# Kernel optimization log

Measured on AMD Instinct MI355X. Metric: run time of the kernel, lower is better.

Reference implementation:

```python
import jax, jax.numpy as jnp
import numpy as np

EPS = 1e-6


def layernorm(x, g, b):
    m = jnp.mean(x, axis=-1, keepdims=True)
    v = jnp.var(x, axis=-1, keepdims=True)
    return (x - m) * jax.lax.rsqrt(v + EPS) * g + b


def dwconv(x, w, b):
    # x: (B,H,W,C), w: (kh,kw,1,C) depthwise kernel, SAME padding (stride 1)
    y = jax.lax.conv_general_dilated(
        x, w, window_strides=(1, 1), padding='SAME',
        dimension_numbers=('NHWC', 'HWIO', 'NHWC'),
        feature_group_count=x.shape[-1])
    return y + b


def setup_inputs() -> dict:
    key = jax.random.key(0)
    ks = jax.random.split(key, 16)
    B, H, W, C = 16, 64, 64, 256
    N, F = 8, 1024
    s = 0.02
    return {
        'x': jax.random.normal(ks[0], (B, H, W, C), jnp.float32),
        'mask_h': jax.random.normal(ks[1], (N, H, H), jnp.float32),
        'mask_w': jax.random.normal(ks[2], (N, W, W), jnp.float32),
        'pos_w': jax.random.normal(ks[3], (3, 3, 1, C), jnp.float32) * s,
        'pos_b': jnp.zeros((C,), jnp.float32),
        'ln1_g': jnp.ones((C,), jnp.float32),
        'ln1_b': jnp.zeros((C,), jnp.float32),
        'wq': jax.random.normal(ks[4], (C, C), jnp.float32) * s,
        'bq': jnp.zeros((C,), jnp.float32),
        'wk': jax.random.normal(ks[5], (C, C), jnp.float32) * s,
        'bk': jnp.zeros((C,), jnp.float32),
        'wv': jax.random.normal(ks[6], (C, C), jnp.float32) * s,
        'bv': jnp.zeros((C,), jnp.float32),
        'lepe_w': jax.random.normal(ks[7], (5, 5, 1, C), jnp.float32) * s,
        'lepe_b': jnp.zeros((C,), jnp.float32),
        'wo': jax.random.normal(ks[8], (C, C), jnp.float32) * s,
        'bo': jnp.zeros((C,), jnp.float32),
        'ln2_g': jnp.ones((C,), jnp.float32),
        'ln2_b': jnp.zeros((C,), jnp.float32),
        'fc1_w': jax.random.normal(ks[9], (C, F), jnp.float32) * s,
        'fc1_b': jnp.zeros((F,), jnp.float32),
        'fc2_w': jax.random.normal(ks[10], (F, C), jnp.float32) * s,
        'fc2_b': jnp.zeros((C,), jnp.float32),
    }


NUM_HEADS = 8


def masad(x, mask_h, mask_w, wq, bq, wk, bk, wv, bv, lepe_w, lepe_b, wo, bo):
    # x: (B,H,W,C); decomposed axial retention (MaSAd)
    B, H, W, C = x.shape
    n = NUM_HEADS
    d = C // n
    scaling = d ** (-0.5)
    q = x @ wq + bq
    k = (x @ wk + bk) * scaling
    v = x @ wv + bv
    lepe = dwconv(v, lepe_w, lepe_b)  # (B,H,W,C)
    q5 = q.reshape(B, H, W, n, d)
    k5 = k.reshape(B, H, W, n, d)
    v5 = v.reshape(B, H, W, n, d)
    # --- W-axis attention: scores (B,H,n,W,W)
    qk_w = jnp.einsum('bhqnd,bhknd->bhnqk', q5, k5)
    Aw = jax.nn.softmax(qk_w + mask_w[None, None], axis=-1)
    vo = jnp.einsum('bhnqk,bhknd->bhqnd', Aw, v5)  # (B,H,W,n,d)
    # --- H-axis attention: scores (B,W,n,H,H)
    qk_h = jnp.einsum('bqwnd,bkwnd->bwnqk', q5, k5)
    Ah = jax.nn.softmax(qk_h + mask_h[None, None], axis=-1)
    out = jnp.einsum('bwnqk,bkwnd->bqwnd', Ah, vo)  # (B,H,W,n,d)
    out = out.reshape(B, H, W, C) + lepe
    return out @ wo + bo


def reference(x, mask_h, mask_w, pos_w, pos_b, ln1_g, ln1_b,
              wq, bq, wk, bk, wv, bv, lepe_w, lepe_b, wo, bo,
              ln2_g, ln2_b, fc1_w, fc1_b, fc2_w, fc2_b):
    x = x + dwconv(x, pos_w, pos_b)
    x = x + masad(layernorm(x, ln1_g, ln1_b), mask_h, mask_w,
                  wq, bq, wk, bk, wv, bv, lepe_w, lepe_b, wo, bo)
    h = layernorm(x, ln2_g, ln2_b)
    h = jax.nn.gelu(h @ fc1_w + fc1_b, approximate=False)
    x = x + (h @ fc2_w + fc2_b)
    return x
```

## Files before the change

kernel.cpp:

```cpp
#include <hip/hip_runtime.h>
#include <hip/hip_bf16.h>
#include <math.h>

typedef unsigned short u16;
typedef unsigned int   u32;
typedef float f4   __attribute__((ext_vector_type(4)));
typedef float f32x4 __attribute__((ext_vector_type(4)));
typedef __bf16 bf16x8 __attribute__((ext_vector_type(8)));

#define BDIM 16
#define HDIM 64
#define WDIM 64
#define CDIM 256
#define NHEAD 8
#define DHEAD 32
#define FDIM 1024
#define MROWS (BDIM*HDIM*WDIM)

__device__ inline float blo(u32 u){ return __uint_as_float(u << 16); }
__device__ inline float bhi(u32 u){ return __uint_as_float(u & 0xffff0000u); }

__device__ inline u16 f2bf(float f){
    __bf16 h = (__bf16)f;
    return __builtin_bit_cast(unsigned short, h);
}
__device__ inline __bf16 u2b(u16 x){ return __builtin_bit_cast(__bf16, x); }
__device__ inline u32 pack2(float lo, float hi){
    return (u32)f2bf(lo) | ((u32)f2bf(hi) << 16);
}
__device__ inline void unp8(uint4 u, float* d){
    d[0]=blo(u.x); d[1]=bhi(u.x); d[2]=blo(u.y); d[3]=bhi(u.y);
    d[4]=blo(u.z); d[5]=bhi(u.z); d[6]=blo(u.w); d[7]=bhi(u.w);
}
__device__ inline void gld16(const void* g, void* l){
    __builtin_amdgcn_global_load_lds(
        (const __attribute__((address_space(1))) void*)g,
        (__attribute__((address_space(3))) void*)l, 16, 0, 0);
}

__global__ __launch_bounds__(256)
void convert_weights_kernel(const float* __restrict__ wq, const float* __restrict__ wk,
                            const float* __restrict__ wv, const float* __restrict__ wo,
                            const float* __restrict__ fc1, const float* __restrict__ fc2,
                            u16* __restrict__ wT)
{
    int i = blockIdx.x * 256 + threadIdx.x;
    const float* src; int K, N, off;
    if (i < 262144) {
        int m = i >> 16;
        src = (m==0) ? wq : (m==1) ? wk : (m==2) ? wv : wo;
        K = 256; N = 256; off = i & 65535;
    } else if (i < 524288) {
        src = fc1; K = 256; N = 1024; off = i - 262144;
    } else {
        src = fc2; K = 1024; N = 256; off = i - 524288;
    }
    int k = off % K, n = off / K;
    wT[i] = f2bf(src[(size_t)k * N + n]);
}

__global__ __launch_bounds__(256)
void posconv_kernel(const float* __restrict__ x, const float* __restrict__ w,
                    const float* __restrict__ bias, float* __restrict__ out)
{
    int idx = blockIdx.x * 256 + threadIdx.x;
    int c = (idx & 63) * 4;
    int p = idx >> 6;
    int wp = p & 63, hp = (p >> 6) & 63, bp = p >> 12;
    f4 acc = *reinterpret_cast<const f4*>(bias + c);
    #pragma unroll
    for (int kh = 0; kh < 3; kh++){
        int hh = hp + kh - 1; if ((unsigned)hh >= 64u) continue;
        #pragma unroll
        for (int kw = 0; kw < 3; kw++){
            int ww = wp + kw - 1; if ((unsigned)ww >= 64u) continue;
            f4 xv = *reinterpret_cast<const f4*>(x + (((size_t)(bp*64 + hh))*64 + ww)*256 + c);
            f4 wv = *reinterpret_cast<const f4*>(w + (size_t)(kh*3 + kw)*256 + c);
            acc += xv * wv;
        }
    }
    f4 ctr = *reinterpret_cast<const f4*>(x + (size_t)p*256 + c);
    *reinterpret_cast<f4*>(out + (size_t)p*256 + c) = ctr + acc;
}

__global__ __launch_bounds__(256)
void lepe_kernel(const u16* __restrict__ v, const float* __restrict__ w,
                 const float* __restrict__ bias, u16* __restrict__ out)
{
    int idx = blockIdx.x * 256 + threadIdx.x;
    int c = (idx & 31) * 8;
    int p = idx >> 5;
    int wp = p & 63, hp = (p >> 6) & 63, bp = p >> 12;
    float acc[8];
    #pragma unroll
    for (int j = 0; j < 8; j++) acc[j] = bias[c + j];
    #pragma unroll
    for (int kh = 0; kh < 5; kh++){
        int hh = hp + kh - 2; if ((unsigned)hh >= 64u) continue;
        #pragma unroll
        for (int kw = 0; kw < 5; kw++){
            int ww = wp + kw - 2; if ((unsigned)ww >= 64u) continue;
            uint4 u = *reinterpret_cast<const uint4*>(v + (((size_t)(bp*64 + hh))*64 + ww)*256 + c);
            float xv[8]; unp8(u, xv);
            const float* wr = w + (size_t)(kh*5 + kw)*256 + c;
            #pragma unroll
            for (int j = 0; j < 8; j++) acc[j] += xv[j] * wr[j];
        }
    }
    uint4 r;
    r.x = pack2(acc[0],acc[1]); r.y = pack2(acc[2],acc[3]);
    r.z = pack2(acc[4],acc[5]); r.w = pack2(acc[6],acc[7]);
    *reinterpret_cast<uint4*>(out + (size_t)p*256 + c) = r;
}

__global__ __launch_bounds__(256)
void ln_kernel(const float* __restrict__ x, const float* __restrict__ g,
               const float* __restrict__ b, u16* __restrict__ y)
{
    int wid = threadIdx.x >> 6, lane = threadIdx.x & 63;
    size_t row = (size_t)blockIdx.x * 4 + wid;
    f4 v = reinterpret_cast<const f4*>(x + row*256)[lane];
    float s  = v.x + v.y + v.z + v.w;
    float q2 = v.x*v.x + v.y*v.y + v.z*v.z + v.w*v.w;
    #pragma unroll
    for (int off = 32; off > 0; off >>= 1){
        s  += __shfl_xor(s,  off);
        q2 += __shfl_xor(q2, off);
    }
    float mean = s * (1.f/256.f);
    float var  = q2 * (1.f/256.f) - mean*mean;
    float rs   = rsqrtf(var + 1e-6f);
    f4 gv = reinterpret_cast<const f4*>(g)[lane];
    f4 bv = reinterpret_cast<const f4*>(b)[lane];
    f4 t = (v - mean) * rs;
    t = t * gv + bv;
    uint2 r;
    r.x = pack2(t.x, t.y); r.y = pack2(t.z, t.w);
    *reinterpret_cast<uint2*>(y + row*256 + (size_t)lane*4) = r;
}

template<int EPI>
__global__ __launch_bounds__(256, 2)
void gemm128_kernel(const u16* __restrict__ A, const u16* __restrict__ Bt,
                    const float* __restrict__ bias, const float* __restrict__ resid,
                    void* __restrict__ outp, int M, int N, int K, float scale)
{
    __shared__ u16 smem[16896];
    u16* As = smem;
    u16* Bs = smem + 8192;
    const int tid = threadIdx.x;
    const int wv = tid >> 6, lane = tid & 63;
    const int g = lane >> 4, lm = lane & 15;
    const int wr = wv >> 1, wc = wv & 1;
    const int n0 = blockIdx.x * 128, m0 = blockIdx.y * 128;

    const int srow  = lane >> 3;
    const int sslot = (lane & 7) ^ srow;

    f32x4 acc[4][4] = {};

    for (int k0 = 0; k0 < K; k0 += 64){
        #pragma unroll
        for (int i = 0; i < 4; i++){
            int rb = wv*32 + i*8;
            gld16(A  + (size_t)(m0 + rb + srow) * K + k0 + sslot*8, &As[rb*64]);
            gld16(Bt + (size_t)(n0 + rb + srow) * K + k0 + sslot*8, &Bs[rb*64]);
        }
        __syncthreads();
        #pragma unroll
        for (int ks = 0; ks < 2; ks++){
            bf16x8 av[4], bv[4];
            #pragma unroll
            for (int mt = 0; mt < 4; mt++){
                int row = wr*64 + mt*16 + lm;
                av[mt] = *reinterpret_cast<const bf16x8*>(&As[row*64 + ((ks*4+g) ^ (row&7))*8]);
            }
            #pragma unroll
            for (int nt = 0; nt < 4; nt++){
                int col = wc*64 + nt*16 + lm;
                bv[nt] = *reinterpret_cast<const bf16x8*>(&Bs[col*64 + ((ks*4+g) ^ (col&7))*8]);
            }
            #pragma unroll
            for (int mt = 0; mt < 4; mt++)
                #pragma unroll
                for (int nt = 0; nt < 4; nt++)
                    acc[mt][nt] = __builtin_amdgcn_mfma_f32_16x16x32_bf16(av[mt], bv[nt], acc[mt][nt], 0, 0, 0);
        }
        __syncthreads();
    }

    if constexpr (EPI == 3){
        #pragma unroll
        for (int nt = 0; nt < 4; nt++){
            int col = n0 + wc*64 + nt*16 + lm;
            float bc = bias[col];
            #pragma unroll
            for (int mt = 0; mt < 4; mt++){
                #pragma unroll
                for (int r = 0; r < 4; r++){
                    int row = m0 + wr*64 + mt*16 + g*4 + r;
                    size_t o = (size_t)row * N + col;
                    reinterpret_cast<float*>(outp)[o] = acc[mt][nt][r] + bc + resid[o];
                }
            }
        }
    } else {
        #pragma unroll
        for (int nt = 0; nt < 4; nt++){
            int col = wc*64 + nt*16 + lm;
            float bc = bias[n0 + col];
            #pragma unroll
            for (int mt = 0; mt < 4; mt++){
                #pragma unroll
                for (int r = 0; r < 4; r++){
                    int row = wr*64 + mt*16 + g*4 + r;
                    float val = acc[mt][nt][r] + bc;
                    if constexpr (EPI == 1) val *= scale;
                    if constexpr (EPI == 2) val = 0.5f * val * (1.f + erff(val * 0.70710678118654752f));
                    smem[row*132 + col] = f2bf(val);
                }
            }
        }
        __syncthreads();
        const int rr = tid >> 4, cs = (tid & 15) * 8;
        #pragma unroll
        for (int pass = 0; pass < 8; pass++){
            int row = pass*16 + rr;
            uint4 u = *reinterpret_cast<const uint4*>(&smem[row*132 + cs]);
            *reinterpret_cast<uint4*>(reinterpret_cast<u16*>(outp) + (size_t)(m0+row)*N + n0 + cs) = u;
        }
    }
}

template<bool HAXIS>
__global__ __launch_bounds__(512, 2)
void attn_mfma_kernel(const u16* __restrict__ q, const u16* __restrict__ k,
                      const u16* __restrict__ v, const float* __restrict__ mask,
                      const u16* __restrict__ lep, u16* __restrict__ out)
{
    __shared__ u16 Kl[8][64][40];
    __shared__ u16 Vl[8][64][34];
    __shared__ u16 Pl[8][64][72];
    u16* Ol = &Pl[0][0][0];

    const int tid = threadIdx.x;
    const int lane = tid & 63, wv = tid >> 6;
    const int g = lane >> 4, lm = lane & 15;

    size_t base, RS;
    if constexpr (HAXIS){
        base = (size_t)(blockIdx.x >> 6) * 1048576 + (size_t)(blockIdx.x & 63) * 256;
        RS = 16384;
    } else {
        base = (size_t)blockIdx.x * 16384;
        RS = 256;
    }

    #pragma unroll
    for (int rnd = 0; rnd < 4; rnd++){
        int c = rnd*512 + tid;
        int kk = c >> 5, hd = (c >> 2) & 7, dh = c & 3;
        size_t gco = base + (size_t)kk*RS + hd*32 + dh*8;
        uint4 uk = *reinterpret_cast<const uint4*>(k + gco);
        *reinterpret_cast<uint4*>(&Kl[hd][kk][dh*8]) = uk;
        uint4 uv = *reinterpret_cast<const uint4*>(v + gco);
        *reinterpret_cast<uint4*>(&Vl[hd][kk][dh*8]) = uv;
    }
    bf16x8 qf[4];
    #pragma unroll
    for (int tj = 0; tj < 4; tj++)
        qf[tj] = *reinterpret_cast<const bf16x8*>(q + base + (size_t)(tj*16+lm)*RS + wv*32 + g*8);
    __syncthreads();

    f32x4 st[4][4];
    #pragma unroll
    for (int ti = 0; ti < 4; ti++){
        bf16x8 kf = *reinterpret_cast<const bf16x8*>(&Kl[wv][ti*16+lm][g*8]);
        #pragma unroll
        for (int tj = 0; tj < 4; tj++){
            f32x4 z = {};
            st[ti][tj] = __builtin_amdgcn_mfma_f32_16x16x32_bf16(kf, qf[tj], z, 0, 0, 0);
        }
    }
    #pragma unroll
    for (int tj = 0; tj < 4; tj++){
        const float* mrow = mask + ((size_t)wv*64 + tj*16+lm)*64;
        #pragma unroll
        for (int ti = 0; ti < 4; ti++)
            st[ti][tj] += *reinterpret_cast<const f4*>(mrow + ti*16 + g*4);
    }
    #pragma unroll
    for (int tj = 0; tj < 4; tj++){
        float mx = -1e30f;
        #pragma unroll
        for (int ti = 0; ti < 4; ti++)
            #pragma unroll
            for (int r = 0; r < 4; r++) mx = fmaxf(mx, st[ti][tj][r]);
        mx = fmaxf(mx, __shfl_xor(mx, 16));
        mx = fmaxf(mx, __shfl_xor(mx, 32));
        float sum = 0.f;
        #pragma unroll
        for (int ti = 0; ti < 4; ti++)
            #pragma unroll
            for (int r = 0; r < 4; r++){
                float p = __expf(st[ti][tj][r] - mx);
                st[ti][tj][r] = p; sum += p;
            }
        sum += __shfl_xor(sum, 16);
        sum += __shfl_xor(sum, 32);
        float inv = 1.f / sum;
        #pragma unroll
        for (int ti = 0; ti < 4; ti++){
            uint2 pw;
            pw.x = pack2(st[ti][tj][0]*inv, st[ti][tj][1]*inv);
            pw.y = pack2(st[ti][tj][2]*inv, st[ti][tj][3]*inv);
            *reinterpret_cast<uint2*>(&Pl[wv][tj*16+lm][ti*16+g*4]) = pw;
        }
    }
    f32x4 oc[4][2] = {};
    #pragma unroll
    for (int kb = 0; kb < 2; kb++){
        bf16x8 vf[2];
        #pragma unroll
        for (int dt = 0; dt < 2; dt++)
            #pragma unroll
            for (int j = 0; j < 8; j++)
                vf[dt][j] = u2b(Vl[wv][kb*32 + g*8 + j][dt*16 + lm]);
        #pragma unroll
        for (int ti2 = 0; ti2 < 4; ti2++){
            bf16x8 pf = *reinterpret_cast<const bf16x8*>(&Pl[wv][ti2*16+lm][kb*32 + g*8]);
            oc[ti2][0] = __builtin_amdgcn_mfma_f32_16x16x32_bf16(pf, vf[0], oc[ti2][0], 0, 0, 0);
            oc[ti2][1] = __builtin_amdgcn_mfma_f32_16x16x32_bf16(pf, vf[1], oc[ti2][1], 0, 0, 0);
        }
    }
    __syncthreads();
    #pragma unroll
    for (int ti2 = 0; ti2 < 4; ti2++)
        #pragma unroll
        for (int dt = 0; dt < 2; dt++)
            #pragma unroll
            for (int r = 0; r < 4; r++)
                Ol[((size_t)wv*64 + ti2*16 + g*4 + r)*40 + dt*16 + lm] = f2bf(oc[ti2][dt][r]);
    __syncthreads();
    #pragma unroll
    for (int rnd = 0; rnd < 4; rnd++){
        int c = rnd*512 + tid;
        int row = c >> 5, hd = (c >> 2) & 7, dh = c & 3;
        uint4 u = *reinterpret_cast<const uint4*>(&Ol[((size_t)hd*64 + row)*40 + dh*8]);
        size_t gco = base + (size_t)row*RS + hd*32 + dh*8;
        if constexpr (HAXIS){
            uint4 ul = *reinterpret_cast<const uint4*>(lep + gco);
            float a[8], b2[8]; unp8(u, a); unp8(ul, b2);
            u.x = pack2(a[0]+b2[0], a[1]+b2[1]);
            u.y = pack2(a[2]+b2[2], a[3]+b2[3]);
            u.z = pack2(a[4]+b2[4], a[5]+b2[5]);
            u.w = pack2(a[6]+b2[6], a[7]+b2[7]);
        }
        *reinterpret_cast<uint4*>(out + gco) = u;
    }
}

extern "C" void kernel_launch(void* const* d_in, const int* in_sizes, int n_in,
                              void* d_out, int out_size, void* d_ws, size_t ws_size,
                              hipStream_t stream)
{
    const float* x      = (const float*)d_in[0];
    const float* mask_h = (const float*)d_in[1];
    const float* mask_w = (const float*)d_in[2];
    const float* pos_w  = (const float*)d_in[3];
    const float* pos_b  = (const float*)d_in[4];
    const float* ln1_g  = (const float*)d_in[5];
    const float* ln1_b  = (const float*)d_in[6];
    const float* wq     = (const float*)d_in[7];
    const float* bq     = (const float*)d_in[8];
    const float* wk     = (const float*)d_in[9];
    const float* bk     = (const float*)d_in[10];
    const float* wv     = (const float*)d_in[11];
    const float* bv     = (const float*)d_in[12];
    const float* lepe_w = (const float*)d_in[13];
    const float* lepe_b = (const float*)d_in[14];
    const float* wo     = (const float*)d_in[15];
    const float* bo     = (const float*)d_in[16];
    const float* ln2_g  = (const float*)d_in[17];
    const float* ln2_b  = (const float*)d_in[18];
    const float* fc1_w  = (const float*)d_in[19];
    const float* fc1_b  = (const float*)d_in[20];
    const float* fc2_w  = (const float*)d_in[21];
    const float* fc2_b  = (const float*)d_in[22];

    const size_t MB = 1u << 20;
    float* x1 = (float*)d_out;

    int Bc = 1;
    for (int c = 16; c >= 1; c >>= 1){
        if (ws_size >= (2 + 10 * (size_t)c) * MB) { Bc = c; break; }
    }

    char* ws = (char*)d_ws;
    u16* wT  = (u16*)ws;
    u16* wqT = wT, *wkT = wT + 65536, *wvT = wT + 131072, *woT = wT + 196608;
    u16* fc1T = wT + 262144, *fc2T = wT + 524288;
    size_t cb = (size_t)Bc * 2 * MB;
    u16* y   = (u16*)(ws + 2*MB);
    u16* qb  = (u16*)(ws + 2*MB + cb);
    u16* kb  = (u16*)(ws + 2*MB + 2*cb);
    u16* vb  = (u16*)(ws + 2*MB + 3*cb);
    u16* lep = (u16*)(ws + 2*MB + 4*cb);
    u16* hb  = qb;

    dim3 blk(256);
    convert_weights_kernel<<<3072, blk, 0, stream>>>(wq, wk, wv, wo, fc1_w, fc2_w, wT);
    posconv_kernel<<<16384, blk, 0, stream>>>(x, pos_w, pos_b, x1);

    const int nchunk = 16 / Bc;
    const int R = Bc * 4096;
    for (int c = 0; c < nchunk; c++){
        float* xc = x1 + (size_t)c * R * 256;
        dim3 gq(2, R/128), gf(8, R/128);
        ln_kernel<<<R/4, blk, 0, stream>>>(xc, ln1_g, ln1_b, y);
        gemm128_kernel<0><<<gq, blk, 0, stream>>>(y, wqT, bq, nullptr, qb, R, 256, 256, 1.f);
        gemm128_kernel<1><<<gq, blk, 0, stream>>>(y, wkT, bk, nullptr, kb, R, 256, 256, 0.17677669529663687f);
        gemm128_kernel<0><<<gq, blk, 0, stream>>>(y, wvT, bv, nullptr, vb, R, 256, 256, 1.f);
        lepe_kernel<<<Bc*512, blk, 0, stream>>>(vb, lepe_w, lepe_b, lep);
        attn_mfma_kernel<false><<<Bc*64, 512, 0, stream>>>(qb, kb, vb, mask_w, nullptr, vb);
        attn_mfma_kernel<true ><<<Bc*64, 512, 0, stream>>>(qb, kb, vb, mask_h, lep, vb);
        gemm128_kernel<3><<<gq, blk, 0, stream>>>(vb, woT, bo, xc, (void*)xc, R, 256, 256, 1.f);
        ln_kernel<<<R/4, blk, 0, stream>>>(xc, ln2_g, ln2_b, y);
        gemm128_kernel<2><<<gf, blk, 0, stream>>>(y, fc1T, fc1_b, nullptr, hb, R, 1024, 256, 1.f);
        gemm128_kernel<3><<<gq, blk, 0, stream>>>(hb, fc2T, fc2_b, xc, (void*)xc, R, 256, 1024, 1.f);
    }
}
```

Baseline: 648.5 us.

## Fuse QKV projections into one GEMM, fuse posconv with LN1, remap GEMM blocks

After: 590.5 us. 8.9% less time.

```diff
diff --git a/kernel.cpp b/kernel.cpp
--- a/kernel.cpp
+++ b/kernel.cpp
@@ -42,29 +42,39 @@
 void convert_weights_kernel(const float* __restrict__ wq, const float* __restrict__ wk,
                             const float* __restrict__ wv, const float* __restrict__ wo,
                             const float* __restrict__ fc1, const float* __restrict__ fc2,
-                            u16* __restrict__ wT)
+                            const float* __restrict__ bq, const float* __restrict__ bk,
+                            const float* __restrict__ bv,
+                            u16* __restrict__ wT, float* __restrict__ bqkv)
 {
     int i = blockIdx.x * 256 + threadIdx.x;
-    const float* src; int K, N, off;
-    if (i < 262144) {
-        int m = i >> 16;
-        src = (m==0) ? wq : (m==1) ? wk : (m==2) ? wv : wo;
-        K = 256; N = 256; off = i & 65535;
-    } else if (i < 524288) {
-        src = fc1; K = 256; N = 1024; off = i - 262144;
+    const float SCL = 0.17677669529663687f;
+    if (i < 786432){
+        const float* src; int K, N, off; float s = 1.f;
+        if (i < 262144){
+            int m = i >> 16;
+            src = (m==0) ? wq : (m==1) ? wk : (m==2) ? wv : wo;
+            if (m == 1) s = SCL;
+            K = 256; N = 256; off = i & 65535;
+        } else if (i < 524288){ src = fc1; K = 256; N = 1024; off = i - 262144; }
+        else                  { src = fc2; K = 1024; N = 256; off = i - 524288; }
+        int k = off % K, n = off / K;
+        wT[i] = f2bf(src[(size_t)k * N + n] * s);
     } else {
-        src = fc2; K = 1024; N = 256; off = i - 524288;
-    }
-    int k = off % K, n = off / K;
-    wT[i] = f2bf(src[(size_t)k * N + n]);
+        int j = i - 786432;
+        if (j < 768)
+            bqkv[j] = (j < 256) ? bq[j] : (j < 512) ? bk[j-256]*SCL : bv[j-512];
+    }
 }
 
 __global__ __launch_bounds__(256)
-void posconv_kernel(const float* __restrict__ x, const float* __restrict__ w,
-                    const float* __restrict__ bias, float* __restrict__ out)
+void posconv_ln1_kernel(const float* __restrict__ x, const float* __restrict__ w,
+                        const float* __restrict__ bias,
+                        const float* __restrict__ lg, const float* __restrict__ lb,
+                        float* __restrict__ x1, u16* __restrict__ y)
 {
     int idx = blockIdx.x * 256 + threadIdx.x;
-    int c = (idx & 63) * 4;
+    int lane = threadIdx.x & 63;
+    int c = lane * 4;
     int p = idx >> 6;
     int wp = p & 63, hp = (p >> 6) & 63, bp = p >> 12;
     f4 acc = *reinterpret_cast<const f4*>(bias + c);
@@ -80,11 +90,28 @@
         }
     }
     f4 ctr = *reinterpret_cast<const f4*>(x + (size_t)p*256 + c);
-    *reinterpret_cast<f4*>(out + (size_t)p*256 + c) = ctr + acc;
+    f4 v = ctr + acc;
+    *reinterpret_cast<f4*>(x1 + (size_t)p*256 + c) = v;
+    float s  = v.x + v.y + v.z + v.w;
+    float q2 = v.x*v.x + v.y*v.y + v.z*v.z + v.w*v.w;
+    #pragma unroll
+    for (int off = 32; off > 0; off >>= 1){
+        s  += __shfl_xor(s,  off);
+        q2 += __shfl_xor(q2, off);
+    }
+    float mean = s * (1.f/256.f);
+    float var  = q2 * (1.f/256.f) - mean*mean;
+    float rs   = rsqrtf(var + 1e-6f);
+    f4 gv = reinterpret_cast<const f4*>(lg)[lane];
+    f4 bv = reinterpret_cast<const f4*>(lb)[lane];
+    f4 t = (v - mean) * rs * gv + bv;
+    uint2 r;
+    r.x = pack2(t.x, t.y); r.y = pack2(t.z, t.w);
+    *reinterpret_cast<uint2*>(y + (size_t)p*256 + (size_t)lane*4) = r;
 }
 
 __global__ __launch_bounds__(256)
-void lepe_kernel(const u16* __restrict__ v, const float* __restrict__ w,
+void lepe_kernel(const u16* __restrict__ qkv, const float* __restrict__ w,
                  const float* __restrict__ bias, u16* __restrict__ out)
 {
     int idx = blockIdx.x * 256 + threadIdx.x;
@@ -100,7 +127,8 @@
         #pragma unroll
         for (int kw = 0; kw < 5; kw++){
             int ww = wp + kw - 2; if ((unsigned)ww >= 64u) continue;
-            uint4 u = *reinterpret_cast<const uint4*>(v + (((size_t)(bp*64 + hh))*64 + ww)*256 + c);
+            uint4 u = *reinterpret_cast<const uint4*>(
+                qkv + (((size_t)(bp*64 + hh))*64 + ww)*768 + 512 + c);
             float xv[8]; unp8(u, xv);
             const float* wr = w + (size_t)(kh*5 + kw)*256 + c;
             #pragma unroll
@@ -141,9 +169,9 @@
 
 template<int EPI>
 __global__ __launch_bounds__(256, 2)
-void gemm128_kernel(const u16* __restrict__ A, const u16* __restrict__ Bt,
+void gemm128_kernel(const u16* __restrict__ A, int lda, const u16* __restrict__ Bt,
                     const float* __restrict__ bias, const float* __restrict__ resid,
-                    void* __restrict__ outp, int M, int N, int K, float scale)
+                    void* __restrict__ outp, int M, int N, int K)
 {
     __shared__ u16 smem[16896];
     u16* As = smem;
@@ -152,7 +180,12 @@
     const int wv = tid >> 6, lane = tid & 63;
     const int g = lane >> 4, lm = lane & 15;
     const int wr = wv >> 1, wc = wv & 1;
-    const int n0 = blockIdx.x * 128, m0 = blockIdx.y * 128;
+
+    int nbx = gridDim.x;
+    int wg = blockIdx.y * nbx + blockIdx.x;
+    int cpx = (nbx * gridDim.y) >> 3;
+    wg = (wg & 7) * cpx + (wg >> 3);
+    const int n0 = (wg % nbx) * 128, m0 = (wg / nbx) * 128;
 
     const int srow  = lane >> 3;
     const int sslot = (lane & 7) ^ srow;
@@ -163,8 +196,8 @@
         #pragma unroll
         for (int i = 0; i < 4; i++){
             int rb = wv*32 + i*8;
-            gld16(A  + (size_t)(m0 + rb + srow) * K + k0 + sslot*8, &As[rb*64]);
-            gld16(Bt + (size_t)(n0 + rb + srow) * K + k0 + sslot*8, &Bs[rb*64]);
+            gld16(A  + (size_t)(m0 + rb + srow) * lda + k0 + sslot*8, &As[rb*64]);
+            gld16(Bt + (size_t)(n0 + rb + srow) * K   + k0 + sslot*8, &Bs[rb*64]);
         }
         __syncthreads();
         #pragma unroll
@@ -215,7 +248,6 @@
                 for (int r = 0; r < 4; r++){
                     int row = wr*64 + mt*16 + g*4 + r;
                     float val = acc[mt][nt][r] + bc;
-                    if constexpr (EPI == 1) val *= scale;
                     if constexpr (EPI == 2) val = 0.5f * val * (1.f + erff(val * 0.70710678118654752f));
                     smem[row*132 + col] = f2bf(val);
                 }
@@ -234,9 +266,8 @@
 
 template<bool HAXIS>
 __global__ __launch_bounds__(512, 2)
-void attn_mfma_kernel(const u16* __restrict__ q, const u16* __restrict__ k,
-                      const u16* __restrict__ v, const float* __restrict__ mask,
-                      const u16* __restrict__ lep, u16* __restrict__ out)
+void attn_mfma_kernel(u16* __restrict__ qkv, const float* __restrict__ mask,
+                      const u16* __restrict__ lep)
 {
     __shared__ u16 Kl[8][64][40];
     __shared__ u16 Vl[8][64][34];
@@ -247,20 +278,26 @@
     const int lane = tid & 63, wv = tid >> 6;
     const int g = lane >> 4, lm = lane & 15;
 
-    size_t base, RS;
+    size_t base, RS, lbase = 0, LRS = 0;
     if constexpr (HAXIS){
-        base = (size_t)(blockIdx.x >> 6) * 1048576 + (size_t)(blockIdx.x & 63) * 256;
-        RS = 16384;
+        int b = blockIdx.x >> 6, wcc = blockIdx.x & 63;
+        base  = (size_t)b * 3145728 + (size_t)wcc * 768;
+        RS    = 49152;
+        lbase = (size_t)b * 1048576 + (size_t)wcc * 256;
+        LRS   = 16384;
     } else {
-        base = (size_t)blockIdx.x * 16384;
-        RS = 256;
-    }
+        base = (size_t)blockIdx.x * 49152;
+        RS   = 768;
+    }
+    const u16* q = qkv + base;
+    const u16* k = qkv + base + 256;
+    u16* v = qkv + base + 512;
 
     #pragma unroll
     for (int rnd = 0; rnd < 4; rnd++){
         int c = rnd*512 + tid;
         int kk = c >> 5, hd = (c >> 2) & 7, dh = c & 3;
-        size_t gco = base + (size_t)kk*RS + hd*32 + dh*8;
+        size_t gco = (size_t)kk*RS + hd*32 + dh*8;
         uint4 uk = *reinterpret_cast<const uint4*>(k + gco);
         *reinterpret_cast<uint4*>(&Kl[hd][kk][dh*8]) = uk;
         uint4 uv = *reinterpret_cast<const uint4*>(v + gco);
@@ -269,7 +306,7 @@
     bf16x8 qf[4];
     #pragma unroll
     for (int tj = 0; tj < 4; tj++)
-        qf[tj] = *reinterpret_cast<const bf16x8*>(q + base + (size_t)(tj*16+lm)*RS + wv*32 + g*8);
+        qf[tj] = *reinterpret_cast<const bf16x8*>(q + (size_t)(tj*16+lm)*RS + wv*32 + g*8);
     __syncthreads();
 
     f32x4 st[4][4];
@@ -347,16 +384,15 @@
         int c = rnd*512 + tid;
         int row = c >> 5, hd = (c >> 2) & 7, dh = c & 3;
         uint4 u = *reinterpret_cast<const uint4*>(&Ol[((size_t)hd*64 + row)*40 + dh*8]);
-        size_t gco = base + (size_t)row*RS + hd*32 + dh*8;
         if constexpr (HAXIS){
-            uint4 ul = *reinterpret_cast<const uint4*>(lep + gco);
+            uint4 ul = *reinterpret_cast<const uint4*>(lep + lbase + (size_t)row*LRS + hd*32 + dh*8);
             float a[8], b2[8]; unp8(u, a); unp8(ul, b2);
             u.x = pack2(a[0]+b2[0], a[1]+b2[1]);
             u.y = pack2(a[2]+b2[2], a[3]+b2[3]);
             u.z = pack2(a[4]+b2[4], a[5]+b2[5]);
             u.w = pack2(a[6]+b2[6], a[7]+b2[7]);
         }
-        *reinterpret_cast<uint4*>(out + gco) = u;
+        *reinterpret_cast<uint4*>(v + (size_t)row*RS + hd*32 + dh*8) = u;
     }
 }
 
@@ -397,36 +433,34 @@
     }
 
     char* ws = (char*)d_ws;
-    u16* wT  = (u16*)ws;
-    u16* wqT = wT, *wkT = wT + 65536, *wvT = wT + 131072, *woT = wT + 196608;
+    u16* wT   = (u16*)ws;
+    float* bqkv = (float*)(ws + 1600*1024);
+    u16* woT  = wT + 196608;
     u16* fc1T = wT + 262144, *fc2T = wT + 524288;
     size_t cb = (size_t)Bc * 2 * MB;
-    u16* y   = (u16*)(ws + 2*MB);
-    u16* qb  = (u16*)(ws + 2*MB + cb);
-    u16* kb  = (u16*)(ws + 2*MB + 2*cb);
-    u16* vb  = (u16*)(ws + 2*MB + 3*cb);
-    u16* lep = (u16*)(ws + 2*MB + 4*cb);
-    u16* hb  = qb;
+    u16* y    = (u16*)(ws + 2*MB);
+    u16* qkvb = (u16*)(ws + 2*MB + cb);
+    u16* lepb = (u16*)(ws + 2*MB + 4*cb);
+    u16* hb   = qkvb;
 
     dim3 blk(256);
-    convert_weights_kernel<<<3072, blk, 0, stream>>>(wq, wk, wv, wo, fc1_w, fc2_w, wT);
-    posconv_kernel<<<16384, blk, 0, stream>>>(x, pos_w, pos_b, x1);
+    convert_weights_kernel<<<3073, blk, 0, stream>>>(wq, wk, wv, wo, fc1_w, fc2_w,
+                                                     bq, bk, bv, wT, bqkv);
 
     const int nchunk = 16 / Bc;
     const int R = Bc * 4096;
     for (int c = 0; c < nchunk; c++){
+        const float* xin = x + (size_t)c * R * 256;
         float* xc = x1 + (size_t)c * R * 256;
-        dim3 gq(2, R/128), gf(8, R/128);
-        ln_kernel<<<R/4, blk, 0, stream>>>(xc, ln1_g, ln1_b, y);
-        gemm128_kernel<0><<<gq, blk, 0, stream>>>(y, wqT, bq, nullptr, qb, R, 256, 256, 1.f);
-        gemm128_kernel<1><<<gq, blk, 0, stream>>>(y, wkT, bk, nullptr, kb, R, 256, 256, 0.17677669529663687f);
-        gemm128_kernel<0><<<gq, blk, 0, stream>>>(y, wvT, bv, nullptr, vb, R, 256, 256, 1.f);
-        lepe_kernel<<<Bc*512, blk, 0, stream>>>(vb, lepe_w, lepe_b, lep);
-        attn_mfma_kernel<false><<<Bc*64, 512, 0, stream>>>(qb, kb, vb, mask_w, nullptr, vb);
-        attn_mfma_kernel<true ><<<Bc*64, 512, 0, stream>>>(qb, kb, vb, mask_h, lep, vb);
-        gemm128_kernel<3><<<gq, blk, 0, stream>>>(vb, woT, bo, xc, (void*)xc, R, 256, 256, 1.f);
+        dim3 gqkv(6, R/128), gq(2, R/128), gf(8, R/128);
+        posconv_ln1_kernel<<<R/4, blk, 0, stream>>>(xin, pos_w, pos_b, ln1_g, ln1_b, xc, y);
+        gemm128_kernel<0><<<gqkv, blk, 0, stream>>>(y, 256, wT, bqkv, nullptr, qkvb, R, 768, 256);
+        lepe_kernel<<<Bc*512, blk, 0, stream>>>(qkvb, lepe_w, lepe_b, lepb);
+        attn_mfma_kernel<false><<<Bc*64, 512, 0, stream>>>(qkvb, mask_w, nullptr);
+        attn_mfma_kernel<true ><<<Bc*64, 512, 0, stream>>>(qkvb, mask_h, lepb);
+        gemm128_kernel<3><<<gq, blk, 0, stream>>>(qkvb + 512, 768, woT, bo, xc, (void*)xc, R, 256, 256);
         ln_kernel<<<R/4, blk, 0, stream>>>(xc, ln2_g, ln2_b, y);
-        gemm128_kernel<2><<<gf, blk, 0, stream>>>(y, fc1T, fc1_b, nullptr, hb, R, 1024, 256, 1.f);
-        gemm128_kernel<3><<<gq, blk, 0, stream>>>(hb, fc2T, fc2_b, xc, (void*)xc, R, 256, 1024, 1.f);
-    }
-}
+        gemm128_kernel<2><<<gf, blk, 0, stream>>>(y, 256, fc1T, fc1_b, nullptr, hb, R, 1024, 256);
+        gemm128_kernel<3><<<gq, blk, 0, stream>>>(hb, 1024, fc2T, fc2_b, xc, (void*)xc, R, 256, 1024);
+    }
+}
```
